# Optimization experiments

Measured on AMD Instinct MI355X. Metric: run time of the kernel, lower is better.

## Reference

```python
import jax, jax.numpy as jnp
import numpy as np

N_NODES = 50000
N_EDGES = 600000
EMB_DIM = 128
NUM_LAYERS = 5
NUM_ELEM = 118
NUM_CHIR = 4
NUM_BOND_TYPE = 4
NUM_BOND_DIR = 3
BN_EPS = 1e-5


def _xavier(key, shape):
    fan_in, fan_out = shape[0], shape[1]
    limit = np.sqrt(6.0 / (fan_in + fan_out))
    return jax.random.uniform(key, shape, jnp.float32, -limit, limit)


def setup_inputs() -> dict:
    key = jax.random.key(0)
    ks = jax.random.split(key, 12)
    x = jax.random.randint(ks[0], (N_NODES, 2), 0, 4, dtype=jnp.int64)
    edge_index = jax.random.randint(ks[1], (2, N_EDGES), 0, N_NODES, dtype=jnp.int64)
    edge_attr = jax.random.randint(ks[2], (N_EDGES, 2), 0, 3, dtype=jnp.int64)
    elem_emb = _xavier(ks[3], (NUM_ELEM, EMB_DIM))
    chir_emb = _xavier(ks[4], (NUM_CHIR, EMB_DIM))
    bond_type_emb = _xavier(ks[5], (NUM_BOND_TYPE, EMB_DIM))
    bond_dir_emb = _xavier(ks[6], (NUM_BOND_DIR, EMB_DIM))
    # shared GINEConv MLP: Linear(D, 2D) -> ReLU -> Linear(2D, D)
    W1 = _xavier(ks[7], (EMB_DIM, 2 * EMB_DIM))
    b1 = jnp.zeros((2 * EMB_DIM,), jnp.float32)
    W2 = _xavier(ks[8], (2 * EMB_DIM, EMB_DIM))
    b2 = jnp.zeros((EMB_DIM,), jnp.float32)
    # per-layer BatchNorm affine params
    bn_gamma = jnp.ones((NUM_LAYERS, EMB_DIM), jnp.float32)
    bn_beta = jnp.zeros((NUM_LAYERS, EMB_DIM), jnp.float32)
    return {
        "x": x, "edge_index": edge_index, "edge_attr": edge_attr,
        "elem_emb": elem_emb, "chir_emb": chir_emb,
        "bond_type_emb": bond_type_emb, "bond_dir_emb": bond_dir_emb,
        "W1": W1, "b1": b1, "W2": W2, "b2": b2,
        "bn_gamma": bn_gamma, "bn_beta": bn_beta,
    }


def reference(x, edge_index, edge_attr, elem_emb, chir_emb,
              bond_type_emb, bond_dir_emb, W1, b1, W2, b2,
              bn_gamma, bn_beta):
    # input embeddings
    h = elem_emb[x[:, 0]] + chir_emb[x[:, 1]]                    # [N, D]
    e = bond_type_emb[edge_attr[:, 0]] + bond_dir_emb[edge_attr[:, 1]]  # [E, D]
    src, dst = edge_index[0], edge_index[1]
    n = h.shape[0]
    num_layers = bn_gamma.shape[0]
    for layer in range(num_layers):  # conv weights shared across layers
        # GINEConv: msg = relu(x_j + edge_attr), scatter-add, eps=0
        msg = jax.nn.relu(h[src] + e)                            # [E, D]
        agg = jax.ops.segment_sum(msg, dst, num_segments=n)      # [N, D]
        z = h + agg
        out = jax.nn.relu(z @ W1 + b1) @ W2 + b2                 # [N, D]
        # BatchNorm1d (training mode: batch stats, biased variance)
        mean = out.mean(axis=0)
        var = out.var(axis=0)
        out = (out - mean) * jax.lax.rsqrt(var + BN_EPS) * bn_gamma[layer] + bn_beta[layer]
        h = out if layer == num_layers - 1 else jax.nn.relu(out)
    return h
```

## Files before the change

kernel.cpp:

```cpp
#include <hip/hip_runtime.h>

typedef _Float16 f16;
typedef _Float16 f16x8 __attribute__((ext_vector_type(8)));
typedef _Float16 h2 __attribute__((ext_vector_type(2)));
typedef float f32x4 __attribute__((ext_vector_type(4)));
typedef unsigned short u16;
typedef unsigned int u32;

__device__ __forceinline__ float bf2f(u16 b) {
  union { u32 u; float f; } t; t.u = ((u32)b) << 16; return t.f;
}
__device__ __forceinline__ u16 f2bf(float f) {
  union { float f; u32 u; } t; t.f = f;
  u32 u = t.u;
  return (u16)((u + 0x7FFFu + ((u >> 16) & 1u)) >> 16);
}
__device__ __forceinline__ u16 f2h_bits(float f) {
  f16 h = (f16)f;
  union { f16 h; u16 u; } t; t.h = h; return t.u;
}
__device__ __forceinline__ float2 up2(u32 p) {
  union { u32 u; f16 h[2]; } t; t.u = p;
  float2 r; r.x = (float)t.h[0]; r.y = (float)t.h[1]; return r;
}
__device__ __forceinline__ u32 pk2(float x, float y) {
  return (u32)f2h_bits(x) | ((u32)f2h_bits(y) << 16);
}
__device__ __forceinline__ h2 asH2(u32 u) {
  union { u32 u; h2 h; } t; t.u = u; return t.h;
}
__device__ __forceinline__ h2 relu2(h2 a) {
#if __has_builtin(__builtin_elementwise_max)
  h2 z = {(_Float16)0, (_Float16)0};
  return __builtin_elementwise_max(a, z);
#else
  h2 r;
  r.x = a.x > (_Float16)0 ? a.x : (_Float16)0;
  r.y = a.y > (_Float16)0 ? a.y : (_Float16)0;
  return r;
#endif
}

__global__ void k_detect(const u16* __restrict__ elemRaw, const int* __restrict__ eiRaw,
                         int* __restrict__ dflags) {
  __shared__ int bad, nzOdd;
  if (threadIdx.x == 0) { bad = 0; nzOdd = 0; }
  __syncthreads();
  int myBad = 0;
  for (int i = threadIdx.x; i < 4096; i += 256) {
    float v = bf2f(elemRaw[i]);
    if (!(v > -0.2f && v < 0.2f)) myBad++;
  }
  if (myBad) atomicAdd(&bad, myBad);
  int myNz = 0;
  for (int i = threadIdx.x; i < 1024; i += 256)
    if (eiRaw[2 * i + 1] != 0) myNz++;
  if (myNz) atomicAdd(&nzOdd, myNz);
  __syncthreads();
  if (threadIdx.x == 0) {
    dflags[0] = (bad == 0) ? 1 : 0;
    dflags[1] = (nzOdd > 16) ? 1 : 0;
  }
}

__global__ void k_init(const u16* __restrict__ elemRaw, const int* __restrict__ eiRaw,
                       int* __restrict__ dflags, int* __restrict__ counts,
                       float* __restrict__ statsC, int NPad, int statsZ) {
  if (blockIdx.x == 0) {
    __shared__ int bad, nzOdd;
    if (threadIdx.x == 0) { bad = 0; nzOdd = 0; }
    __syncthreads();
    int myBad = 0;
    for (int i = threadIdx.x; i < 4096; i += 256) {
      float v = bf2f(elemRaw[i]);
      if (!(v > -0.2f && v < 0.2f)) myBad++;
    }
    if (myBad) atomicAdd(&bad, myBad);
    int myNz = 0;
    for (int i = threadIdx.x; i < 1024; i += 256)
      if (eiRaw[2 * i + 1] != 0) myNz++;
    if (myNz) atomicAdd(&nzOdd, myNz);
    __syncthreads();
    if (threadIdx.x == 0) {
      dflags[0] = (bad == 0) ? 1 : 0;
      dflags[1] = (nzOdd > 16) ? 1 : 0;
    }
  } else {
    int i = (blockIdx.x - 1) * 256 + threadIdx.x;
    if (i < NPad) counts[i] = 0;
    else if (i < NPad + statsZ) statsC[i - NPad] = 0.f;
  }
}

__global__ void k_canary(u32* __restrict__ out, const int* __restrict__ dflags,
                         int out_size, u32 pBf, u32 pF32) {
  int isbf = dflags[0];
  int words = isbf ? (out_size >> 1) : out_size;
  int i = blockIdx.x * 256 + threadIdx.x;
  if (i < words) out[i] = isbf ? pBf : pF32;
}

__global__ void k_cvt(const int* __restrict__ xR, const int* __restrict__ eiR,
                      const int* __restrict__ eaR,
                      const u16* e0, const u16* e1, const u16* e2, const u16* e3,
                      const u16* e4, const u16* e5, const u16* e6, const u16* e7,
                      const u16* e8, const u16* e9,
                      const int* __restrict__ dflags,
                      int* __restrict__ x32, int* __restrict__ ei32, int* __restrict__ combo,
                      int* __restrict__ counts, float* __restrict__ dst,
                      int N, int E, int intBlocks) {
  if ((int)blockIdx.x < intBlocks) {
    int pi = blockIdx.x * 256 + threadIdx.x;
    int nPairs = N + 2 * E;
    if (pi >= nPairs) return;
    int is32 = dflags[1];
    const int* src; int local; int kind;
    if (pi < N) { src = xR; local = pi; kind = 0; }
    else if (pi < N + E) { src = eiR; local = pi - N; kind = 1; }
    else { src = eaR; local = pi - N - E; kind = 2; }
    int j0 = 2 * local;
    int v0, v1;
    if (is32) { int2 v = *(const int2*)(src + j0); v0 = v.x; v1 = v.y; }
    else      { int4 v = *(const int4*)(src + 2 * j0); v0 = v.x; v1 = v.z; }
    if (kind == 0) { x32[j0] = v0; x32[j0 + 1] = v1; }
    else if (kind == 1) {
      ei32[j0] = v0; ei32[j0 + 1] = v1;
      if (j0 >= E) {
        atomicAdd(&counts[v0], 1);
        atomicAdd(&counts[v1], 1);
      }
    } else {
      combo[local] = v0 * 3 + v1;
    }
  } else {
    int i = (blockIdx.x - intBlocks) * 256 + threadIdx.x;
    if (i >= 83712) return;
    int isbf = dflags[0];
    const u16* src; int j;
    if      (i < 15104) { src = e0; j = i; }
    else if (i < 15616) { src = e1; j = i - 15104; }
    else if (i < 16128) { src = e2; j = i - 15616; }
    else if (i < 16512) { src = e3; j = i - 16128; }
    else if (i < 49280) { src = e4; j = i - 16512; }
    else if (i < 49536) { src = e5; j = i - 49280; }
    else if (i < 82304) { src = e6; j = i - 49536; }
    else if (i < 82432) { src = e7; j = i - 82304; }
    else if (i < 83072) { src = e8; j = i - 82432; }
    else                { src = e9; j = i - 83072; }
    dst[i] = isbf ? bf2f(src[j]) : ((const float*)src)[j];
  }
}

__global__ void k_chunksum(const int* __restrict__ counts, int* __restrict__ bsum) {
  int tid = threadIdx.x, lane = tid & 63, w = tid >> 6;
  const int4* c4 = (const int4*)(counts + blockIdx.x * 1024);
  int4 v = c4[tid];
  int s = v.x + v.y + v.z + v.w;
#pragma unroll
  for (int d = 1; d < 64; d <<= 1) s += __shfl_xor(s, d);
  __shared__ int ws[4];
  if (lane == 0) ws[w] = s;
  __syncthreads();
  if (tid == 0) bsum[blockIdx.x] = ws[0] + ws[1] + ws[2] + ws[3];
}

__global__ void k_chunkscan(const int* __restrict__ bsum, int* __restrict__ boff,
                            int* __restrict__ row_start, int N, int nCh) {
  int t = threadIdx.x;
  int v = (t < nCh) ? bsum[t] : 0;
  int incl = v;
#pragma unroll
  for (int d = 1; d < 64; d <<= 1) { int tmp = __shfl_up(incl, d); if (t >= d) incl += tmp; }
  boff[t] = incl - v;
  if (t == 63) row_start[N] = incl;
}

__global__ void k_scanapply(const int* __restrict__ counts, const int* __restrict__ boff,
                            int* __restrict__ row_start, int* __restrict__ cursor, int N) {
  int tid = threadIdx.x, lane = tid & 63, w = tid >> 6;
  int base = blockIdx.x * 1024 + tid * 4;
  int4 v = *(const int4*)(counts + base);
  int tsum = v.x + v.y + v.z + v.w;
  int incl = tsum;
#pragma unroll
  for (int d = 1; d < 64; d <<= 1) { int tmp = __shfl_up(incl, d); if (lane >= d) incl += tmp; }
  __shared__ int ws[4];
  if (lane == 63) ws[w] = incl;
  __syncthreads();
  int woff = 0;
  for (int j = 0; j < w; ++j) woff += ws[j];
  int excl = boff[blockIdx.x] + woff + incl - tsum;
  int e0 = excl, e1 = excl + v.x, e2 = e1 + v.y, e3 = e2 + v.z;
  if (base < N)     { row_start[base] = e0;     cursor[base] = e0; }
  if (base + 1 < N) { row_start[base + 1] = e1; cursor[base + 1] = e1; }
  if (base + 2 < N) { row_start[base + 2] = e2; cursor[base + 2] = e2; }
  if (base + 3 < N) { row_start[base + 3] = e3; cursor[base + 3] = e3; }
}

__global__ void k_scatter(const int* __restrict__ ei, const int* __restrict__ combo,
                          int* cursor, int* packed, int E) {
  int e = blockIdx.x * blockDim.x + threadIdx.x;
  if (e >= E) return;
  int s = ei[e], d = ei[E + e];
  int cb = combo[e];
  int pos = atomicAdd(&cursor[d], 1);
  packed[pos] = s | (cb << 20);
}

__global__ void k_prep(const float* __restrict__ cflt, const int* __restrict__ x,
                       u32* __restrict__ W1F, u32* __restrict__ W2F,
                       u32* __restrict__ tblC, u32* __restrict__ hb, int N, int wtBlocks) {
  if ((int)blockIdx.x < wtBlocks) {
    const float* W1 = cflt + 16512;
    const float* W2 = cflt + 49536;
    const float* bt = cflt + 15616;
    const float* bd = cflt + 16128;
    int g = blockIdx.x * 256 + threadIdx.x;
    {
      int e = g >> 2, wd = g & 3;
      int lane = e & 63, nt = (e >> 6) & 3, ks = (e >> 8) & 3, c = (e >> 10) & 3;
      int q = lane >> 4, lo = lane & 15;
      int n = c * 64 + nt * 16 + lo;
      int k0 = (ks * 4 + q) * 8 + wd * 2;
      W1F[g] = pk2(W1[k0 * 256 + n], W1[(k0 + 1) * 256 + n]);
    }
    {
      int e = g >> 2, wd = g & 3;
      int lane = e & 63, nt = (e >> 6) & 7, ks2 = (e >> 9) & 1, c = (e >> 10) & 3;
      int q = lane >> 4, lo = lane & 15;
      int n2 = nt * 16 + lo;
      int k20 = c * 64 + (ks2 * 4 + q) * 8 + wd * 2;
      W2F[g] = pk2(W2[k20 * 128 + n2], W2[(k20 + 1) * 128 + n2]);
    }
    if (g < 768) {
      int combo = g >> 6, l = g & 63, c0 = l * 2;
      int a0 = combo / 3, a1 = combo - a0 * 3;
      tblC[g] = pk2(bt[a0 * 128 + c0] + bd[a1 * 128 + c0],
                    bt[a0 * 128 + c0 + 1] + bd[a1 * 128 + c0 + 1]);
    }
  } else {
    const float* elem = cflt;
    const float* chir = cflt + 15104;
    int b = blockIdx.x - wtBlocks;
    int wv = (int)(threadIdx.x >> 6);
    int lane = threadIdx.x & 63;
    int node = b * 4 + wv;
    if (node >= N) return;
    int x0 = x[node * 2], x1 = x[node * 2 + 1];
    int c0 = lane * 2;
    float vx = elem[x0 * 128 + c0] + chir[x1 * 128 + c0];
    float vy = elem[x0 * 128 + c0 + 1] + chir[x1 * 128 + c0 + 1];
    hb[(size_t)node * 64 + lane] = pk2(vx, vy);
  }
}

__global__ __launch_bounds__(256) void k_agg(
    const u32* __restrict__ hb, const int* __restrict__ row_start,
    const int* __restrict__ packed, const u32* __restrict__ tblC,
    u32* __restrict__ z, int N) {
  __shared__ u32 tbl[768];
  for (int idx = threadIdx.x; idx < 768; idx += 256) tbl[idx] = tblC[idx];
  __syncthreads();
  const uint4* tbl4 = (const uint4*)tbl;
  const int tid = threadIdx.x;
  const int w = tid >> 6, lane = tid & 63;
  const int sub = lane >> 4, li = lane & 15;
  const int node = blockIdx.x * 16 + w * 4 + sub;
  if (node >= N) return;
  const uint4* hb4 = (const uint4*)hb;
  uint4 sv = hb4[(size_t)node * 16 + li];
  float2 s0 = up2(sv.x), s1 = up2(sv.y), s2 = up2(sv.z), s3 = up2(sv.w);
  float ax0 = s0.x, ay0 = s0.y, ax1 = s1.x, ay1 = s1.y;
  float ax2 = s2.x, ay2 = s2.y, ax3 = s3.x, ay3 = s3.y;
  const int s_ = row_start[node], e_ = row_start[node + 1];
  int p = s_;
  for (; p + 4 <= e_; p += 4) {
    int k0 = packed[p], k1 = packed[p + 1], k2 = packed[p + 2], k3 = packed[p + 3];
    uint4 r0 = hb4[(size_t)(k0 & 0xFFFFF) * 16 + li];
    uint4 r1 = hb4[(size_t)(k1 & 0xFFFFF) * 16 + li];
    uint4 r2 = hb4[(size_t)(k2 & 0xFFFFF) * 16 + li];
    uint4 r3 = hb4[(size_t)(k3 & 0xFFFFF) * 16 + li];
    uint4 t0 = tbl4[(k0 >> 20) * 16 + li];
    uint4 t1 = tbl4[(k1 >> 20) * 16 + li];
    uint4 t2 = tbl4[(k2 >> 20) * 16 + li];
    uint4 t3 = tbl4[(k3 >> 20) * 16 + li];
    h2 m;
    m = relu2(asH2(r0.x) + asH2(t0.x)); ax0 += (float)m.x; ay0 += (float)m.y;
    m = relu2(asH2(r0.y) + asH2(t0.y)); ax1 += (float)m.x; ay1 += (float)m.y;
    m = relu2(asH2(r0.z) + asH2(t0.z)); ax2 += (float)m.x; ay2 += (float)m.y;
    m = relu2(asH2(r0.w) + asH2(t0.w)); ax3 += (float)m.x; ay3 += (float)m.y;
    m = relu2(asH2(r1.x) + asH2(t1.x)); ax0 += (float)m.x; ay0 += (float)m.y;
    m = relu2(asH2(r1.y) + asH2(t1.y)); ax1 += (float)m.x; ay1 += (float)m.y;
    m = relu2(asH2(r1.z) + asH2(t1.z)); ax2 += (float)m.x; ay2 += (float)m.y;
    m = relu2(asH2(r1.w) + asH2(t1.w)); ax3 += (float)m.x; ay3 += (float)m.y;
    m = relu2(asH2(r2.x) + asH2(t2.x)); ax0 += (float)m.x; ay0 += (float)m.y;
    m = relu2(asH2(r2.y) + asH2(t2.y)); ax1 += (float)m.x; ay1 += (float)m.y;
    m = relu2(asH2(r2.z) + asH2(t2.z)); ax2 += (float)m.x; ay2 += (float)m.y;
    m = relu2(asH2(r2.w) + asH2(t2.w)); ax3 += (float)m.x; ay3 += (float)m.y;
    m = relu2(asH2(r3.x) + asH2(t3.x)); ax0 += (float)m.x; ay0 += (float)m.y;
    m = relu2(asH2(r3.y) + asH2(t3.y)); ax1 += (float)m.x; ay1 += (float)m.y;
    m = relu2(asH2(r3.z) + asH2(t3.z)); ax2 += (float)m.x; ay2 += (float)m.y;
    m = relu2(asH2(r3.w) + asH2(t3.w)); ax3 += (float)m.x; ay3 += (float)m.y;
  }
  for (; p < e_; ++p) {
    int k0 = packed[p];
    uint4 r0 = hb4[(size_t)(k0 & 0xFFFFF) * 16 + li];
    uint4 t0 = tbl4[(k0 >> 20) * 16 + li];
    h2 m;
    m = relu2(asH2(r0.x) + asH2(t0.x)); ax0 += (float)m.x; ay0 += (float)m.y;
    m = relu2(asH2(r0.y) + asH2(t0.y)); ax1 += (float)m.x; ay1 += (float)m.y;
    m = relu2(asH2(r0.z) + asH2(t0.z)); ax2 += (float)m.x; ay2 += (float)m.y;
    m = relu2(asH2(r0.w) + asH2(t0.w)); ax3 += (float)m.x; ay3 += (float)m.y;
  }
  uint4 o;
  o.x = pk2(ax0, ay0); o.y = pk2(ax1, ay1); o.z = pk2(ax2, ay2); o.w = pk2(ax3, ay3);
  ((uint4*)z)[(size_t)node * 16 + li] = o;
}

__global__ __launch_bounds__(512, 2) void k_mlp(
    const u16* __restrict__ z, const u32* __restrict__ W1F, const u32* __restrict__ W2F,
    const float* __restrict__ b1, const float* __restrict__ b2,
    u16* __restrict__ act, float* __restrict__ statsC, int N, int nTiles) {
  __shared__ u32 sW1[16384];
  __shared__ u32 sW2[16384];
  __shared__ u16 sYp[8][1024];
  __shared__ float sStats[256];

  const int tid = threadIdx.x;
  const int w = tid >> 6, lane = tid & 63;
  const int lo = lane & 15, q = lane >> 4;

  if (tid < 256) sStats[tid] = 0.f;
  {
    const int4* gW1 = (const int4*)W1F;
    const int4* gW2 = (const int4*)W2F;
    int4* lW1 = (int4*)sW1;
    int4* lW2 = (int4*)sW2;
#pragma unroll
    for (int it = 0; it < 8; ++it) {
      int o = it * 512 + tid;
      lW1[o] = gW1[o];
      lW2[o] = gW2[o];
    }
  }
  __syncthreads();

  float rb1[16], rb2[8];
#pragma unroll
  for (int c = 0; c < 4; ++c)
#pragma unroll
    for (int nt = 0; nt < 4; ++nt)
      rb1[c * 4 + nt] = b1[c * 64 + nt * 16 + lo];
#pragma unroll
  for (int nt = 0; nt < 8; ++nt)
    rb2[nt] = b2[nt * 16 + lo];

  float aSum[8] = {}, aSq[8] = {};
  u16* myY = sYp[w];

  for (int t = blockIdx.x * 8 + w; t < nTiles; t += 2048) {
    const int row0 = t * 16;
    f16x8 a1[4];
    const char* zrow = (const char*)z + (size_t)(row0 + lo) * 256;
#pragma unroll
    for (int ks = 0; ks < 4; ++ks)
      a1[ks] = *(const f16x8*)(zrow + (ks * 4 + q) * 16);

    f32x4 accO[8] = {};
#pragma unroll
    for (int c = 0; c < 4; ++c) {
      f16x8 B1[16];
#pragma unroll
      for (int i = 0; i < 16; ++i)
        B1[i] = *(const f16x8*)((const char*)sW1 + ((c * 16 + i) << 10) + lane * 16);
      f32x4 acc1[4] = {};
#pragma unroll
      for (int ks = 0; ks < 4; ++ks)
#pragma unroll
        for (int nt = 0; nt < 4; ++nt)
          acc1[nt] = __builtin_amdgcn_mfma_f32_16x16x32_f16(a1[ks], B1[ks * 4 + nt], acc1[nt], 0, 0, 0);
#pragma unroll
      for (int nt = 0; nt < 4; ++nt) {
        int ycol = nt * 16 + lo;
        float bias = rb1[c * 4 + nt];
#pragma unroll
        for (int i = 0; i < 4; ++i) {
          int m = q * 4 + i;
          float v = fmaxf(acc1[nt][i] + bias, 0.f);
          myY[m * 64 + (((ycol >> 3) ^ (m & 7)) << 3) + (ycol & 7)] = f2h_bits(v);
        }
      }
      f16x8 B2[16];
#pragma unroll
      for (int i = 0; i < 16; ++i)
        B2[i] = *(const f16x8*)((const char*)sW2 + ((c * 16 + i) << 10) + lane * 16);
#pragma unroll
      for (int ks2 = 0; ks2 < 2; ++ks2) {
        int kq2 = ks2 * 4 + q;
        f16x8 a2 = *(const f16x8*)(myY + lo * 64 + ((kq2 ^ (lo & 7)) << 3));
#pragma unroll
        for (int nt = 0; nt < 8; ++nt)
          accO[nt] = __builtin_amdgcn_mfma_f32_16x16x32_f16(a2, B2[ks2 * 8 + nt], accO[nt], 0, 0, 0);
      }
    }
#pragma unroll
    for (int nt = 0; nt < 8; ++nt) {
      int n2 = nt * 16 + lo;
      float bias = rb2[nt];
#pragma unroll
      for (int i = 0; i < 4; ++i) {
        int row = row0 + q * 4 + i;
        float v = accO[nt][i] + bias;
        act[(size_t)row * 128 + n2] = f2h_bits(v);
        if (row < N) { aSum[nt] += v; aSq[nt] += v * v; }
      }
    }
  }

#pragma unroll
  for (int nt = 0; nt < 8; ++nt) {
    float s = aSum[nt], s2 = aSq[nt];
    s += __shfl_xor(s, 16); s += __shfl_xor(s, 32);
    s2 += __shfl_xor(s2, 16); s2 += __shfl_xor(s2, 32);
    if (q == 0) {
      atomicAdd(&sStats[nt * 16 + lo], s);
      atomicAdd(&sStats[128 + nt * 16 + lo], s2);
    }
  }
  __syncthreads();
  if (tid < 256) atomicAdd(&statsC[(blockIdx.x & 31) * 256 + tid], sStats[tid]);
}

__global__ __launch_bounds__(256) void k_bnapply(
    const u32* __restrict__ act, const float* __restrict__ statsC,
    const float* __restrict__ gamma, const float* __restrict__ beta,
    float invN, u32* __restrict__ hb, int N) {
  __shared__ float sTot[256];
  __shared__ float ssc[128], ssh[128];
  int tid = threadIdx.x;
  {
    float acc = 0.f;
#pragma unroll
    for (int c = 0; c < 32; ++c) acc += statsC[c * 256 + tid];
    sTot[tid] = acc;
  }
  __syncthreads();
  if (tid < 128) {
    float mean = sTot[tid] * invN;
    float var = sTot[128 + tid] * invN - mean * mean;
    float inv = rsqrtf(var + 1e-5f);
    float scv = gamma[tid] * inv;
    ssc[tid] = scv;
    ssh[tid] = beta[tid] - mean * scv;
  }
  __syncthreads();
  int total = N * 64;
  for (int i = blockIdx.x * 256 + tid; i < total; i += gridDim.x * 256) {
    int c0 = (i & 63) * 2;
    float2 v = up2(act[i]);
    float ox = fmaxf(v.x * ssc[c0] + ssh[c0], 0.f);
    float oy = fmaxf(v.y * ssc[c0 + 1] + ssh[c0 + 1], 0.f);
    hb[i] = pk2(ox, oy);
  }
}

__global__ __launch_bounds__(256) void k_final(
    const u32* __restrict__ act, const float* __restrict__ statsC,
    const float* __restrict__ gamma, const float* __restrict__ beta,
    float invN, const int* __restrict__ dflags, void* __restrict__ outv, int N) {
  __shared__ float sTot[256];
  __shared__ float ssc[128], ssh[128];
  int tid = threadIdx.x;
  {
    float acc = 0.f;
#pragma unroll
    for (int c = 0; c < 32; ++c) acc += statsC[c * 256 + tid];
    sTot[tid] = acc;
  }
  __syncthreads();
  if (tid < 128) {
    float mean = sTot[tid] * invN;
    float var = sTot[128 + tid] * invN - mean * mean;
    float inv = rsqrtf(var + 1e-5f);
    float scv = gamma[tid] * inv;
    ssc[tid] = scv;
    ssh[tid] = beta[tid] - mean * scv;
  }
  __syncthreads();
  int isbf = dflags[0];
  int total = N * 64;
  for (int i = blockIdx.x * 256 + tid; i < total; i += gridDim.x * 256) {
    int c0 = (i & 63) * 2;
    float2 v = up2(act[i]);
    float ox = v.x * ssc[c0] + ssh[c0];
    float oy = v.y * ssc[c0 + 1] + ssh[c0 + 1];
    if (isbf) ((u32*)outv)[i] = (u32)f2bf(ox) | ((u32)f2bf(oy) << 16);
    else { float2 o; o.x = ox; o.y = oy; ((float2*)outv)[i] = o; }
  }
}

extern "C" void kernel_launch(void* const* d_in, const int* in_sizes, int n_in,
                              void* d_out, int out_size, void* d_ws, size_t ws_size,
                              hipStream_t stream) {
  const int* xR  = (const int*)d_in[0];
  const int* eiR = (const int*)d_in[1];
  const int* eaR = (const int*)d_in[2];
  const u16* emR = (const u16*)d_in[3];
  const u16* chR = (const u16*)d_in[4];
  const u16* btR = (const u16*)d_in[5];
  const u16* bdR = (const u16*)d_in[6];
  const u16* W1R = (const u16*)d_in[7];
  const u16* b1R = (const u16*)d_in[8];
  const u16* W2R = (const u16*)d_in[9];
  const u16* b2R = (const u16*)d_in[10];
  const u16* gR  = (const u16*)d_in[11];
  const u16* beR = (const u16*)d_in[12];

  const int N = in_sizes[0] / 2;
  const int E = in_sizes[1] / 2;
  const int L = in_sizes[11] / 128;
  const int Mpad = ((N + 63) / 64) * 64;
  const int nCh = (N + 1023) / 1024;
  const int NPad = nCh * 1024;
  const int nTiles = (N + 15) / 16;

  char* base = (char*)d_ws;
  size_t off = 0;
  auto take = [&](size_t bytes) -> void* {
    void* p = base + off;
    off += (bytes + 255) & ~(size_t)255;
    return p;
  };
  int*   dflags    = (int*)  take(256);
  int*   x32       = (int*)  take((size_t)2 * N * 4);
  int*   ei32      = (int*)  take((size_t)2 * E * 4);
  int*   combo     = (int*)  take((size_t)E * 4);
  float* cflt      = (float*)take(83712 * 4);
  u32*   act       = (u32*)  take((size_t)Mpad * 64 * 4);
  u32*   hb        = (u32*)  take((size_t)Mpad * 64 * 4);
  u16*   zb        = (u16*)  take((size_t)Mpad * 128 * 2);
  int*   packed    = (int*)  take((size_t)E * 4);
  int*   row_start = (int*)  take((size_t)(N + 1) * 4);
  int*   cursor    = (int*)  take((size_t)N * 4);
  int*   counts    = (int*)  take((size_t)NPad * 4);
  int*   bsum      = (int*)  take(64 * 4);
  int*   boff      = (int*)  take(64 * 4);
  float* statsC    = (float*)take((size_t)L * 32 * 256 * 4);
  u32*   W1F       = (u32*)  take(16384 * 4);
  u32*   W2F       = (u32*)  take(16384 * 4);
  u32*   tblC      = (u32*)  take(768 * 4);
  const size_t need = off;
  (void)n_in;

  float* cB1 = cflt + 49280;
  float* cB2 = cflt + 82304;
  float* cGamma = cflt + 82432;
  float* cBeta = cflt + 83072;

  if (need > ws_size) {
    k_detect<<<dim3(1), dim3(256), 0, stream>>>(emR, eiR, dflags);
    k_canary<<<dim3((out_size + 255) / 256), dim3(256), 0, stream>>>(
        (u32*)d_out, dflags, out_size, 0x40004000u, 0x40000000u);
    return;
  }

  const int statsZ = L * 32 * 256;
  const int nzBlocks = (NPad + statsZ + 255) / 256;
  k_init<<<dim3(nzBlocks + 1), dim3(256), 0, stream>>>(emR, eiR, dflags, counts, statsC,
                                                       NPad, statsZ);

  const int nPairs = N + 2 * E;
  const int intBlocks = (nPairs + 255) / 256;
  const int fltBlocks = (83712 + 255) / 256;
  k_cvt<<<dim3(intBlocks + fltBlocks), dim3(256), 0, stream>>>(
      xR, eiR, eaR, emR, chR, btR, bdR, W1R, b1R, W2R, b2R, gR, beR,
      dflags, x32, ei32, combo, counts, cflt, N, E, intBlocks);

  k_chunksum<<<dim3(nCh), dim3(256), 0, stream>>>(counts, bsum);
  k_chunkscan<<<dim3(1), dim3(64), 0, stream>>>(bsum, boff, row_start, N, nCh);
  k_scanapply<<<dim3(nCh), dim3(256), 0, stream>>>(counts, boff, row_start, cursor, N);
  k_scatter<<<dim3((E + 255) / 256), dim3(256), 0, stream>>>(ei32, combo, cursor, packed, E);

  const int wtBlocks = 64;
  k_prep<<<dim3(wtBlocks + (N + 3) / 4), dim3(256), 0, stream>>>(
      cflt, x32, W1F, W2F, tblC, hb, N, wtBlocks);

  const float invN = 1.0f / (float)N;
  for (int l = 0; l < L; ++l) {
    k_agg<<<dim3((N + 15) / 16), dim3(256), 0, stream>>>(
        hb, row_start, packed, tblC, (u32*)zb, N);
    k_mlp<<<dim3(256), dim3(512), 0, stream>>>(
        zb, W1F, W2F, cB1, cB2, (u16*)act, statsC + (size_t)l * 32 * 256, N, nTiles);
    if (l < L - 1) {
      k_bnapply<<<dim3(1024), dim3(256), 0, stream>>>(
          act, statsC + (size_t)l * 32 * 256, cGamma + (size_t)l * 128,
          cBeta + (size_t)l * 128, invN, hb, N);
    }
  }
  k_final<<<dim3(1024), dim3(256), 0, stream>>>(
      act, statsC + (size_t)(L - 1) * 32 * 256, cGamma + (size_t)(L - 1) * 128,
      cBeta + (size_t)(L - 1) * 128, invN, dflags, d_out, N);
}
```

Measured before the change: 451.1 us.

## Process aggregation nodes in degree-sorted order to balance per-wave work

```diff
diff --git a/kernel.cpp b/kernel.cpp
--- a/kernel.cpp
+++ b/kernel.cpp
@@ -65,7 +65,8 @@
 
 __global__ void k_init(const u16* __restrict__ elemRaw, const int* __restrict__ eiRaw,
                        int* __restrict__ dflags, int* __restrict__ counts,
-                       float* __restrict__ statsC, int NPad, int statsZ) {
+                       float* __restrict__ statsC, int* __restrict__ dhist,
+                       int NPad, int statsZ) {
   if (blockIdx.x == 0) {
     __shared__ int bad, nzOdd;
     if (threadIdx.x == 0) { bad = 0; nzOdd = 0; }
@@ -89,6 +90,7 @@
     int i = (blockIdx.x - 1) * 256 + threadIdx.x;
     if (i < NPad) counts[i] = 0;
     else if (i < NPad + statsZ) statsC[i - NPad] = 0.f;
+    else if (i < NPad + statsZ + 64) dhist[i - NPad - statsZ] = 0;
   }
 }
 
@@ -151,42 +153,75 @@
   }
 }
 
-__global__ void k_chunksum(const int* __restrict__ counts, int* __restrict__ bsum) {
+__global__ void k_chunksum(const int* __restrict__ counts, int* __restrict__ bsum,
+                           int* __restrict__ dhist, int N) {
   int tid = threadIdx.x, lane = tid & 63, w = tid >> 6;
+  __shared__ int lh[64];
+  __shared__ int ws[4];
+  if (tid < 64) lh[tid] = 0;
+  __syncthreads();
   const int4* c4 = (const int4*)(counts + blockIdx.x * 1024);
   int4 v = c4[tid];
+  int base = blockIdx.x * 1024 + tid * 4;
+  if (base < N)     atomicAdd(&lh[min(v.x, 63)], 1);
+  if (base + 1 < N) atomicAdd(&lh[min(v.y, 63)], 1);
+  if (base + 2 < N) atomicAdd(&lh[min(v.z, 63)], 1);
+  if (base + 3 < N) atomicAdd(&lh[min(v.w, 63)], 1);
   int s = v.x + v.y + v.z + v.w;
 #pragma unroll
   for (int d = 1; d < 64; d <<= 1) s += __shfl_xor(s, d);
+  if (lane == 0) ws[w] = s;
+  __syncthreads();
+  if (tid == 0) bsum[blockIdx.x] = ws[0] + ws[1] + ws[2] + ws[3];
+  if (tid < 64 && lh[tid]) atomicAdd(&dhist[tid], lh[tid]);
+}
+
+__global__ void k_chunkscan(const int* __restrict__ bsum, int* __restrict__ boff,
+                            int* __restrict__ row_start, const int* __restrict__ dhist,
+                            int* __restrict__ dcur, int N, int nCh) {
+  int tid = threadIdx.x;
+  if (tid < 64) {
+    int t = tid;
+    int v = (t < nCh) ? bsum[t] : 0;
+    int incl = v;
+#pragma unroll
+    for (int d = 1; d < 64; d <<= 1) { int tmp = __shfl_up(incl, d); if (t >= d) incl += tmp; }
+    boff[t] = incl - v;
+    if (t == 63) row_start[N] = incl;
+  } else {
+    int t = tid - 64;
+    int v = dhist[t];
+    int incl = v;
+#pragma unroll
+    for (int d = 1; d < 64; d <<= 1) { int tmp = __shfl_up(incl, d); if (t >= d) incl += tmp; }
+    dcur[t] = incl - v;
+  }
+}
+
+__global__ void k_scanapply(const int* __restrict__ counts, const int* __restrict__ boff,
+                            int* __restrict__ row_start, int* __restrict__ cursor,
+                            int* __restrict__ dcur, int* __restrict__ order, int N) {
+  int tid = threadIdx.x, lane = tid & 63, w = tid >> 6;
+  __shared__ int lh[64];
+  __shared__ int lb[64];
   __shared__ int ws[4];
-  if (lane == 0) ws[w] = s;
-  __syncthreads();
-  if (tid == 0) bsum[blockIdx.x] = ws[0] + ws[1] + ws[2] + ws[3];
-}
-
-__global__ void k_chunkscan(const int* __restrict__ bsum, int* __restrict__ boff,
-                            int* __restrict__ row_start, int N, int nCh) {
-  int t = threadIdx.x;
-  int v = (t < nCh) ? bsum[t] : 0;
-  int incl = v;
-#pragma unroll
-  for (int d = 1; d < 64; d <<= 1) { int tmp = __shfl_up(incl, d); if (t >= d) incl += tmp; }
-  boff[t] = incl - v;
-  if (t == 63) row_start[N] = incl;
-}
-
-__global__ void k_scanapply(const int* __restrict__ counts, const int* __restrict__ boff,
-                            int* __restrict__ row_start, int* __restrict__ cursor, int N) {
-  int tid = threadIdx.x, lane = tid & 63, w = tid >> 6;
+  if (tid < 64) lh[tid] = 0;
+  __syncthreads();
   int base = blockIdx.x * 1024 + tid * 4;
   int4 v = *(const int4*)(counts + base);
+  int d0 = min(v.x, 63), d1 = min(v.y, 63), d2 = min(v.z, 63), d3 = min(v.w, 63);
+  int o0 = 0, o1 = 0, o2 = 0, o3 = 0;
+  if (base < N)     o0 = atomicAdd(&lh[d0], 1);
+  if (base + 1 < N) o1 = atomicAdd(&lh[d1], 1);
+  if (base + 2 < N) o2 = atomicAdd(&lh[d2], 1);
+  if (base + 3 < N) o3 = atomicAdd(&lh[d3], 1);
   int tsum = v.x + v.y + v.z + v.w;
   int incl = tsum;
 #pragma unroll
   for (int d = 1; d < 64; d <<= 1) { int tmp = __shfl_up(incl, d); if (lane >= d) incl += tmp; }
-  __shared__ int ws[4];
   if (lane == 63) ws[w] = incl;
   __syncthreads();
+  if (tid < 64) lb[tid] = lh[tid] ? atomicAdd(&dcur[tid], lh[tid]) : 0;
   int woff = 0;
   for (int j = 0; j < w; ++j) woff += ws[j];
   int excl = boff[blockIdx.x] + woff + incl - tsum;
@@ -195,6 +230,11 @@
   if (base + 1 < N) { row_start[base + 1] = e1; cursor[base + 1] = e1; }
   if (base + 2 < N) { row_start[base + 2] = e2; cursor[base + 2] = e2; }
   if (base + 3 < N) { row_start[base + 3] = e3; cursor[base + 3] = e3; }
+  __syncthreads();
+  if (base < N)     order[lb[d0] + o0] = base;
+  if (base + 1 < N) order[lb[d1] + o1] = base + 1;
+  if (base + 2 < N) order[lb[d2] + o2] = base + 2;
+  if (base + 3 < N) order[lb[d3] + o3] = base + 3;
 }
 
 __global__ void k_scatter(const int* __restrict__ ei, const int* __restrict__ combo,
@@ -257,6 +297,7 @@
 __global__ __launch_bounds__(256) void k_agg(
     const u32* __restrict__ hb, const int* __restrict__ row_start,
     const int* __restrict__ packed, const u32* __restrict__ tblC,
+    const int* __restrict__ order,
     u32* __restrict__ z, int N) {
   __shared__ u32 tbl[768];
   for (int idx = threadIdx.x; idx < 768; idx += 256) tbl[idx] = tblC[idx];
@@ -265,8 +306,9 @@
   const int tid = threadIdx.x;
   const int w = tid >> 6, lane = tid & 63;
   const int sub = lane >> 4, li = lane & 15;
-  const int node = blockIdx.x * 16 + w * 4 + sub;
-  if (node >= N) return;
+  const int nidx = blockIdx.x * 16 + w * 4 + sub;
+  if (nidx >= N) return;
+  const int node = order[nidx];
   const uint4* hb4 = (const uint4*)hb;
   uint4 sv = hb4[(size_t)node * 16 + li];
   float2 s0 = up2(sv.x), s1 = up2(sv.y), s2 = up2(sv.z), s3 = up2(sv.w);
@@ -549,6 +591,9 @@
   u32*   W1F       = (u32*)  take(16384 * 4);
   u32*   W2F       = (u32*)  take(16384 * 4);
   u32*   tblC      = (u32*)  take(768 * 4);
+  int*   order     = (int*)  take((size_t)N * 4);
+  int*   dhist     = (int*)  take(64 * 4);
+  int*   dcur      = (int*)  take(64 * 4);
   const size_t need = off;
   (void)n_in;
 
@@ -565,9 +610,9 @@
   }
 
   const int statsZ = L * 32 * 256;
-  const int nzBlocks = (NPad + statsZ + 255) / 256;
+  const int nzBlocks = (NPad + statsZ + 64 + 255) / 256;
   k_init<<<dim3(nzBlocks + 1), dim3(256), 0, stream>>>(emR, eiR, dflags, counts, statsC,
-                                                       NPad, statsZ);
+                                                       dhist, NPad, statsZ);
 
   const int nPairs = N + 2 * E;
   const int intBlocks = (nPairs + 255) / 256;
@@ -576,9 +621,10 @@
       xR, eiR, eaR, emR, chR, btR, bdR, W1R, b1R, W2R, b2R, gR, beR,
       dflags, x32, ei32, combo, counts, cflt, N, E, intBlocks);
 
-  k_chunksum<<<dim3(nCh), dim3(256), 0, stream>>>(counts, bsum);
-  k_chunkscan<<<dim3(1), dim3(64), 0, stream>>>(bsum, boff, row_start, N, nCh);
-  k_scanapply<<<dim3(nCh), dim3(256), 0, stream>>>(counts, boff, row_start, cursor, N);
+  k_chunksum<<<dim3(nCh), dim3(256), 0, stream>>>(counts, bsum, dhist, N);
+  k_chunkscan<<<dim3(1), dim3(128), 0, stream>>>(bsum, boff, row_start, dhist, dcur, N, nCh);
+  k_scanapply<<<dim3(nCh), dim3(256), 0, stream>>>(counts, boff, row_start, cursor,
+                                                   dcur, order, N);
   k_scatter<<<dim3((E + 255) / 256), dim3(256), 0, stream>>>(ei32, combo, cursor, packed, E);
 
   const int wtBlocks = 64;
@@ -588,7 +634,7 @@
   const float invN = 1.0f / (float)N;
   for (int l = 0; l < L; ++l) {
     k_agg<<<dim3((N + 15) / 16), dim3(256), 0, stream>>>(
-        hb, row_start, packed, tblC, (u32*)zb, N);
+        hb, row_start, packed, tblC, order, (u32*)zb, N);
     k_mlp<<<dim3(256), dim3(512), 0, stream>>>(
         zb, W1F, W2F, cB1, cB2, (u16*)act, statsC + (size_t)l * 32 * 256, N, nTiles);
     if (l < L - 1) {
```

Measured after the change: 451.9 us. Within noise of the previous version (+0.2%).

## Fuse per-layer agg, MLP and batchnorm into one cooperative persistent kernel

Applied to the files above, without the earlier changes.

```diff
diff --git a/kernel.cpp b/kernel.cpp
--- a/kernel.cpp
+++ b/kernel.cpp
@@ -1,4 +1,7 @@
 #include <hip/hip_runtime.h>
+#include <hip/hip_cooperative_groups.h>
+
+namespace cg = cooperative_groups;
 
 typedef _Float16 f16;
 typedef _Float16 f16x8 __attribute__((ext_vector_type(8)));
@@ -254,6 +257,225 @@
   }
 }
 
+
+__device__ __forceinline__ void agg_body(
+    const u32* __restrict__ hb, const int* __restrict__ row_start,
+    const int* __restrict__ packed, const uint4* __restrict__ tbl4,
+    u32* __restrict__ z, int N, int bid, int nb, int w, int lane) {
+  const int sub = lane >> 4, li = lane & 15;
+  const uint4* hb4 = (const uint4*)hb;
+#define ACC4(R, T)                                                              \
+  {                                                                             \
+    h2 m;                                                                       \
+    m = relu2(asH2((R).x) + asH2((T).x)); ax0 += (float)m.x; ay0 += (float)m.y; \
+    m = relu2(asH2((R).y) + asH2((T).y)); ax1 += (float)m.x; ay1 += (float)m.y; \
+    m = relu2(asH2((R).z) + asH2((T).z)); ax2 += (float)m.x; ay2 += (float)m.y; \
+    m = relu2(asH2((R).w) + asH2((T).w)); ax3 += (float)m.x; ay3 += (float)m.y; \
+  }
+  for (int base = bid * 32; base < N; base += nb * 32) {
+    const int node = base + w * 4 + sub;
+    if (node >= N) continue;
+    uint4 sv = hb4[(size_t)node * 16 + li];
+    float2 s0 = up2(sv.x), s1 = up2(sv.y), s2 = up2(sv.z), s3 = up2(sv.w);
+    float ax0 = s0.x, ay0 = s0.y, ax1 = s1.x, ay1 = s1.y;
+    float ax2 = s2.x, ay2 = s2.y, ax3 = s3.x, ay3 = s3.y;
+    const int s_ = row_start[node], e_ = row_start[node + 1];
+    int p = s_;
+    for (; p + 4 <= e_; p += 4) {
+      int k0 = packed[p], k1 = packed[p + 1], k2 = packed[p + 2], k3 = packed[p + 3];
+      uint4 r0 = hb4[(size_t)(k0 & 0xFFFFF) * 16 + li];
+      uint4 r1 = hb4[(size_t)(k1 & 0xFFFFF) * 16 + li];
+      uint4 r2 = hb4[(size_t)(k2 & 0xFFFFF) * 16 + li];
+      uint4 r3 = hb4[(size_t)(k3 & 0xFFFFF) * 16 + li];
+      uint4 t;
+      t = tbl4[(k0 >> 20) * 16 + li]; ACC4(r0, t)
+      t = tbl4[(k1 >> 20) * 16 + li]; ACC4(r1, t)
+      t = tbl4[(k2 >> 20) * 16 + li]; ACC4(r2, t)
+      t = tbl4[(k3 >> 20) * 16 + li]; ACC4(r3, t)
+    }
+    for (; p < e_; ++p) {
+      int k0 = packed[p];
+      uint4 r0 = hb4[(size_t)(k0 & 0xFFFFF) * 16 + li];
+      uint4 t = tbl4[(k0 >> 20) * 16 + li];
+      ACC4(r0, t)
+    }
+    uint4 o;
+    o.x = pk2(ax0, ay0); o.y = pk2(ax1, ay1); o.z = pk2(ax2, ay2); o.w = pk2(ax3, ay3);
+    ((uint4*)z)[(size_t)node * 16 + li] = o;
+  }
+#undef ACC4
+}
+
+__global__ __launch_bounds__(512, 1) void k_fused(
+    u32* hb, u32* zb, u32* act,
+    const int* row_start, const int* packed,
+    const u32* tblC, const u32* W1F, const u32* W2F,
+    const float* b1, const float* b2,
+    const float* gamma, const float* beta, float* statsC,
+    const int* dflags, void* outv,
+    int N, int nTiles, int L, float invN) {
+  __shared__ u32 sW1[16384];
+  __shared__ u32 sW2[16384];
+  __shared__ u16 sYp[8][1024];
+  __shared__ float sStats[256];
+  __shared__ u32 tbl[768];
+  __shared__ float ssc[128], ssh[128];
+
+  cg::grid_group grid = cg::this_grid();
+
+  const int tid = threadIdx.x;
+  const int w = tid >> 6, lane = tid & 63;
+  const int lo = lane & 15, q = lane >> 4;
+  const int bid = blockIdx.x, nb = gridDim.x;
+
+  {
+    const int4* gW1 = (const int4*)W1F;
+    const int4* gW2 = (const int4*)W2F;
+    int4* lW1 = (int4*)sW1;
+    int4* lW2 = (int4*)sW2;
+    for (int o = tid; o < 4096; o += 512) { lW1[o] = gW1[o]; lW2[o] = gW2[o]; }
+    for (int idx = tid; idx < 768; idx += 512) tbl[idx] = tblC[idx];
+  }
+  float rb1[16], rb2[8];
+#pragma unroll
+  for (int c = 0; c < 4; ++c)
+#pragma unroll
+    for (int nt = 0; nt < 4; ++nt)
+      rb1[c * 4 + nt] = b1[c * 64 + nt * 16 + lo];
+#pragma unroll
+  for (int nt = 0; nt < 8; ++nt)
+    rb2[nt] = b2[nt * 16 + lo];
+  __syncthreads();
+
+  u16* myY = sYp[w];
+
+  for (int l = 0; l < L; ++l) {
+    agg_body(hb, row_start, packed, (const uint4*)tbl, zb, N, bid, nb, w, lane);
+    grid.sync();
+
+    if (tid < 256) sStats[tid] = 0.f;
+    __syncthreads();
+    {
+      float aSum[8] = {}, aSq[8] = {};
+      const u16* z16 = (const u16*)zb;
+      for (int t = bid * 8 + w; t < nTiles; t += nb * 8) {
+        const int row0 = t * 16;
+        f16x8 a1[4];
+        const char* zrow = (const char*)z16 + (size_t)(row0 + lo) * 256;
+#pragma unroll
+        for (int ks = 0; ks < 4; ++ks)
+          a1[ks] = *(const f16x8*)(zrow + (ks * 4 + q) * 16);
+
+        f32x4 accO[8] = {};
+#pragma unroll
+        for (int c = 0; c < 4; ++c) {
+          f16x8 B1[16];
+#pragma unroll
+          for (int i = 0; i < 16; ++i)
+            B1[i] = *(const f16x8*)((const char*)sW1 + ((c * 16 + i) << 10) + lane * 16);
+          f32x4 acc1[4] = {};
+#pragma unroll
+          for (int ks = 0; ks < 4; ++ks)
+#pragma unroll
+            for (int nt = 0; nt < 4; ++nt)
+              acc1[nt] = __builtin_amdgcn_mfma_f32_16x16x32_f16(a1[ks], B1[ks * 4 + nt], acc1[nt], 0, 0, 0);
+#pragma unroll
+          for (int nt = 0; nt < 4; ++nt) {
+            int ycol = nt * 16 + lo;
+            float bias = rb1[c * 4 + nt];
+#pragma unroll
+            for (int i = 0; i < 4; ++i) {
+              int m = q * 4 + i;
+              float v = fmaxf(acc1[nt][i] + bias, 0.f);
+              myY[m * 64 + (((ycol >> 3) ^ (m & 7)) << 3) + (ycol & 7)] = f2h_bits(v);
+            }
+          }
+          f16x8 B2[16];
+#pragma unroll
+          for (int i = 0; i < 16; ++i)
+            B2[i] = *(const f16x8*)((const char*)sW2 + ((c * 16 + i) << 10) + lane * 16);
+#pragma unroll
+          for (int ks2 = 0; ks2 < 2; ++ks2) {
+            int kq2 = ks2 * 4 + q;
+            f16x8 a2 = *(const f16x8*)(myY + lo * 64 + ((kq2 ^ (lo & 7)) << 3));
+#pragma unroll
+            for (int nt = 0; nt < 8; ++nt)
+              accO[nt] = __builtin_amdgcn_mfma_f32_16x16x32_f16(a2, B2[ks2 * 8 + nt], accO[nt], 0, 0, 0);
+          }
+        }
+#pragma unroll
+        for (int nt = 0; nt < 8; ++nt) {
+          int n2 = nt * 16 + lo;
+          float bias = rb2[nt];
+#pragma unroll
+          for (int i = 0; i < 4; ++i) {
+            int row = row0 + q * 4 + i;
+            float v = accO[nt][i] + bias;
+            ((u16*)act)[(size_t)row * 128 + n2] = f2h_bits(v);
+            if (row < N) { aSum[nt] += v; aSq[nt] += v * v; }
+          }
+        }
+      }
+#pragma unroll
+      for (int nt = 0; nt < 8; ++nt) {
+        float s = aSum[nt], s2 = aSq[nt];
+        s += __shfl_xor(s, 16); s += __shfl_xor(s, 32);
+        s2 += __shfl_xor(s2, 16); s2 += __shfl_xor(s2, 32);
+        if (q == 0) {
+          atomicAdd(&sStats[nt * 16 + lo], s);
+          atomicAdd(&sStats[128 + nt * 16 + lo], s2);
+        }
+      }
+      __syncthreads();
+      float* scl = statsC + (size_t)l * 32 * 256;
+      if (tid < 256) atomicAdd(&scl[(bid & 31) * 256 + tid], sStats[tid]);
+    }
+    grid.sync();
+
+    {
+      const float* scl = statsC + (size_t)l * 32 * 256;
+      if (tid < 256) {
+        float acc = 0.f;
+#pragma unroll
+        for (int c = 0; c < 32; ++c) acc += scl[c * 256 + tid];
+        sStats[tid] = acc;
+      }
+      __syncthreads();
+      if (tid < 128) {
+        float mean = sStats[tid] * invN;
+        float var = sStats[128 + tid] * invN - mean * mean;
+        float inv = rsqrtf(var + 1e-5f);
+        float scv = gamma[l * 128 + tid] * inv;
+        ssc[tid] = scv;
+        ssh[tid] = beta[l * 128 + tid] - mean * scv;
+      }
+      __syncthreads();
+      int total = N * 64;
+      if (l < L - 1) {
+        for (int i = bid * 512 + tid; i < total; i += nb * 512) {
+          int c0 = (i & 63) * 2;
+          float2 v = up2(act[i]);
+          float ox = fmaxf(v.x * ssc[c0] + ssh[c0], 0.f);
+          float oy = fmaxf(v.y * ssc[c0 + 1] + ssh[c0 + 1], 0.f);
+          hb[i] = pk2(ox, oy);
+        }
+        grid.sync();
+      } else {
+        int isbf = dflags[0];
+        for (int i = bid * 512 + tid; i < total; i += nb * 512) {
+          int c0 = (i & 63) * 2;
+          float2 v = up2(act[i]);
+          float ox = v.x * ssc[c0] + ssh[c0];
+          float oy = v.y * ssc[c0 + 1] + ssh[c0 + 1];
+          if (isbf) ((u32*)outv)[i] = (u32)f2bf(ox) | ((u32)f2bf(oy) << 16);
+          else { float2 o2; o2.x = ox; o2.y = oy; ((float2*)outv)[i] = o2; }
+        }
+      }
+    }
+  }
+}
+
+
 __global__ __launch_bounds__(256) void k_agg(
     const u32* __restrict__ hb, const int* __restrict__ row_start,
     const int* __restrict__ packed, const u32* __restrict__ tblC,
@@ -261,60 +483,9 @@
   __shared__ u32 tbl[768];
   for (int idx = threadIdx.x; idx < 768; idx += 256) tbl[idx] = tblC[idx];
   __syncthreads();
-  const uint4* tbl4 = (const uint4*)tbl;
   const int tid = threadIdx.x;
   const int w = tid >> 6, lane = tid & 63;
-  const int sub = lane >> 4, li = lane & 15;
-  const int node = blockIdx.x * 16 + w * 4 + sub;
-  if (node >= N) return;
-  const uint4* hb4 = (const uint4*)hb;
-  uint4 sv = hb4[(size_t)node * 16 + li];
-  float2 s0 = up2(sv.x), s1 = up2(sv.y), s2 = up2(sv.z), s3 = up2(sv.w);
-  float ax0 = s0.x, ay0 = s0.y, ax1 = s1.x, ay1 = s1.y;
-  float ax2 = s2.x, ay2 = s2.y, ax3 = s3.x, ay3 = s3.y;
-  const int s_ = row_start[node], e_ = row_start[node + 1];
-  int p = s_;
-  for (; p + 4 <= e_; p += 4) {
-    int k0 = packed[p], k1 = packed[p + 1], k2 = packed[p + 2], k3 = packed[p + 3];
-    uint4 r0 = hb4[(size_t)(k0 & 0xFFFFF) * 16 + li];
-    uint4 r1 = hb4[(size_t)(k1 & 0xFFFFF) * 16 + li];
-    uint4 r2 = hb4[(size_t)(k2 & 0xFFFFF) * 16 + li];
-    uint4 r3 = hb4[(size_t)(k3 & 0xFFFFF) * 16 + li];
-    uint4 t0 = tbl4[(k0 >> 20) * 16 + li];
-    uint4 t1 = tbl4[(k1 >> 20) * 16 + li];
-    uint4 t2 = tbl4[(k2 >> 20) * 16 + li];
-    uint4 t3 = tbl4[(k3 >> 20) * 16 + li];
-    h2 m;
-    m = relu2(asH2(r0.x) + asH2(t0.x)); ax0 += (float)m.x; ay0 += (float)m.y;
-    m = relu2(asH2(r0.y) + asH2(t0.y)); ax1 += (float)m.x; ay1 += (float)m.y;
-    m = relu2(asH2(r0.z) + asH2(t0.z)); ax2 += (float)m.x; ay2 += (float)m.y;
-    m = relu2(asH2(r0.w) + asH2(t0.w)); ax3 += (float)m.x; ay3 += (float)m.y;
-    m = relu2(asH2(r1.x) + asH2(t1.x)); ax0 += (float)m.x; ay0 += (float)m.y;
-    m = relu2(asH2(r1.y) + asH2(t1.y)); ax1 += (float)m.x; ay1 += (float)m.y;
-    m = relu2(asH2(r1.z) + asH2(t1.z)); ax2 += (float)m.x; ay2 += (float)m.y;
-    m = relu2(asH2(r1.w) + asH2(t1.w)); ax3 += (float)m.x; ay3 += (float)m.y;
-    m = relu2(asH2(r2.x) + asH2(t2.x)); ax0 += (float)m.x; ay0 += (float)m.y;
-    m = relu2(asH2(r2.y) + asH2(t2.y)); ax1 += (float)m.x; ay1 += (float)m.y;
-    m = relu2(asH2(r2.z) + asH2(t2.z)); ax2 += (float)m.x; ay2 += (float)m.y;
-    m = relu2(asH2(r2.w) + asH2(t2.w)); ax3 += (float)m.x; ay3 += (float)m.y;
-    m = relu2(asH2(r3.x) + asH2(t3.x)); ax0 += (float)m.x; ay0 += (float)m.y;
-    m = relu2(asH2(r3.y) + asH2(t3.y)); ax1 += (float)m.x; ay1 += (float)m.y;
-    m = relu2(asH2(r3.z) + asH2(t3.z)); ax2 += (float)m.x; ay2 += (float)m.y;
-    m = relu2(asH2(r3.w) + asH2(t3.w)); ax3 += (float)m.x; ay3 += (float)m.y;
-  }
-  for (; p < e_; ++p) {
-    int k0 = packed[p];
-    uint4 r0 = hb4[(size_t)(k0 & 0xFFFFF) * 16 + li];
-    uint4 t0 = tbl4[(k0 >> 20) * 16 + li];
-    h2 m;
-    m = relu2(asH2(r0.x) + asH2(t0.x)); ax0 += (float)m.x; ay0 += (float)m.y;
-    m = relu2(asH2(r0.y) + asH2(t0.y)); ax1 += (float)m.x; ay1 += (float)m.y;
-    m = relu2(asH2(r0.z) + asH2(t0.z)); ax2 += (float)m.x; ay2 += (float)m.y;
-    m = relu2(asH2(r0.w) + asH2(t0.w)); ax3 += (float)m.x; ay3 += (float)m.y;
-  }
-  uint4 o;
-  o.x = pk2(ax0, ay0); o.y = pk2(ax1, ay1); o.z = pk2(ax2, ay2); o.w = pk2(ax3, ay3);
-  ((uint4*)z)[(size_t)node * 16 + li] = o;
+  agg_body(hb, row_start, packed, (const uint4*)tbl, z, N, blockIdx.x, gridDim.x, w, lane);
 }
 
 __global__ __launch_bounds__(512, 2) void k_mlp(
@@ -533,7 +704,7 @@
   };
   int*   dflags    = (int*)  take(256);
   int*   x32       = (int*)  take((size_t)2 * N * 4);
-  int*   ei32      = (int*)  take((size_t)2 * E * 4);
+  int*   ei32     = (int*)  take((size_t)2 * E * 4);
   int*   combo     = (int*)  take((size_t)E * 4);
   float* cflt      = (float*)take(83712 * 4);
   u32*   act       = (u32*)  take((size_t)Mpad * 64 * 4);
@@ -586,8 +757,36 @@
       cflt, x32, W1F, W2F, tblC, hb, N, wtBlocks);
 
   const float invN = 1.0f / (float)N;
+
+  {
+    u32* zb32 = (u32*)zb;
+    void* outp = d_out;
+    const int* rsC = row_start;
+    const int* pkC = packed;
+    const u32* tblCC = tblC;
+    const u32* W1C = W1F;
+    const u32* W2C = W2F;
+    const float* b1C = cB1;
+    const float* b2C = cB2;
+    const float* gC = cGamma;
+    const float* beC = cBeta;
+    const int* dfC = dflags;
+    int Nv = N, nTv = nTiles, Lv = L;
+    float invNv = invN;
+    void* kargs[] = {
+        (void*)&hb, (void*)&zb32, (void*)&act,
+        (void*)&rsC, (void*)&pkC, (void*)&tblCC, (void*)&W1C, (void*)&W2C,
+        (void*)&b1C, (void*)&b2C, (void*)&gC, (void*)&beC, (void*)&statsC,
+        (void*)&dfC, (void*)&outp,
+        (void*)&Nv, (void*)&nTv, (void*)&Lv, (void*)&invNv};
+    hipError_t err = hipLaunchCooperativeKernel(
+        (void*)k_fused, dim3(256), dim3(512), kargs, 0, stream);
+    if (err == hipSuccess) return;
+    (void)hipGetLastError();
+  }
+
   for (int l = 0; l < L; ++l) {
-    k_agg<<<dim3((N + 15) / 16), dim3(256), 0, stream>>>(
+    k_agg<<<dim3((N + 31) / 32), dim3(256), 0, stream>>>(
         hb, row_start, packed, tblC, (u32*)zb, N);
     k_mlp<<<dim3(256), dim3(512), 0, stream>>>(
         zb, W1F, W2F, cB1, cB2, (u16*)act, statsC + (size_t)l * 32 * 256, N, nTiles);
```

Result: slower. 945.8 us (+109.7%).

## Fuse MLP and BatchNorm apply into one cooperative kernel with grid sync

Applied to the files above, without the earlier changes.

```diff
diff --git a/kernel.cpp b/kernel.cpp
--- a/kernel.cpp
+++ b/kernel.cpp
@@ -1,4 +1,7 @@
 #include <hip/hip_runtime.h>
+#include <hip/hip_cooperative_groups.h>
+
+namespace cg = cooperative_groups;
 
 typedef _Float16 f16;
 typedef _Float16 f16x8 __attribute__((ext_vector_type(8)));
@@ -317,48 +320,13 @@
   ((uint4*)z)[(size_t)node * 16 + li] = o;
 }
 
-__global__ __launch_bounds__(512, 2) void k_mlp(
-    const u16* __restrict__ z, const u32* __restrict__ W1F, const u32* __restrict__ W2F,
-    const float* __restrict__ b1, const float* __restrict__ b2,
-    u16* __restrict__ act, float* __restrict__ statsC, int N, int nTiles) {
-  __shared__ u32 sW1[16384];
-  __shared__ u32 sW2[16384];
-  __shared__ u16 sYp[8][1024];
-  __shared__ float sStats[256];
-
-  const int tid = threadIdx.x;
-  const int w = tid >> 6, lane = tid & 63;
-  const int lo = lane & 15, q = lane >> 4;
-
-  if (tid < 256) sStats[tid] = 0.f;
-  {
-    const int4* gW1 = (const int4*)W1F;
-    const int4* gW2 = (const int4*)W2F;
-    int4* lW1 = (int4*)sW1;
-    int4* lW2 = (int4*)sW2;
-#pragma unroll
-    for (int it = 0; it < 8; ++it) {
-      int o = it * 512 + tid;
-      lW1[o] = gW1[o];
-      lW2[o] = gW2[o];
-    }
-  }
-  __syncthreads();
-
-  float rb1[16], rb2[8];
-#pragma unroll
-  for (int c = 0; c < 4; ++c)
-#pragma unroll
-    for (int nt = 0; nt < 4; ++nt)
-      rb1[c * 4 + nt] = b1[c * 64 + nt * 16 + lo];
-#pragma unroll
-  for (int nt = 0; nt < 8; ++nt)
-    rb2[nt] = b2[nt * 16 + lo];
-
+__device__ __forceinline__ void mlp_body(
+    const u16* __restrict__ z, const u32* sW1, const u32* sW2,
+    const float* rb1, const float* rb2, u16* myY,
+    u16* __restrict__ act, float* sStats, float* __restrict__ statsCl,
+    int N, int nTiles, int bid, int nb, int w, int lane, int lo, int q, int tid) {
   float aSum[8] = {}, aSq[8] = {};
-  u16* myY = sYp[w];
-
-  for (int t = blockIdx.x * 8 + w; t < nTiles; t += 2048) {
+  for (int t = bid * 8 + w; t < nTiles; t += nb * 8) {
     const int row0 = t * 16;
     f16x8 a1[4];
     const char* zrow = (const char*)z + (size_t)(row0 + lo) * 256;
@@ -416,7 +384,6 @@
       }
     }
   }
-
 #pragma unroll
   for (int nt = 0; nt < 8; ++nt) {
     float s = aSum[nt], s2 = aSq[nt];
@@ -428,7 +395,138 @@
     }
   }
   __syncthreads();
-  if (tid < 256) atomicAdd(&statsC[(blockIdx.x & 31) * 256 + tid], sStats[tid]);
+  if (tid < 256) atomicAdd(&statsCl[(bid & 31) * 256 + tid], sStats[tid]);
+}
+
+__global__ __launch_bounds__(512, 1) void k_mlpbn(
+    const u16* z, const u32* W1F, const u32* W2F,
+    const float* b1, const float* b2,
+    u16* act, float* statsCl,
+    const float* gamma, const float* beta, float invN,
+    u32* hb, const int* dflags, void* outv, int isFinal, int N, int nTiles) {
+  __shared__ u32 sW1[16384];
+  __shared__ u32 sW2[16384];
+  __shared__ u16 sYp[8][1024];
+  __shared__ float sStats[256];
+  __shared__ float ssc[128], ssh[128];
+
+  cg::grid_group grid = cg::this_grid();
+
+  const int tid = threadIdx.x;
+  const int w = tid >> 6, lane = tid & 63;
+  const int lo = lane & 15, q = lane >> 4;
+  const int bid = blockIdx.x, nb = gridDim.x;
+
+  if (tid < 256) sStats[tid] = 0.f;
+  {
+    const int4* gW1 = (const int4*)W1F;
+    const int4* gW2 = (const int4*)W2F;
+    int4* lW1 = (int4*)sW1;
+    int4* lW2 = (int4*)sW2;
+#pragma unroll
+    for (int it = 0; it < 8; ++it) {
+      int o = it * 512 + tid;
+      lW1[o] = gW1[o];
+      lW2[o] = gW2[o];
+    }
+  }
+  __syncthreads();
+
+  float rb1[16], rb2[8];
+#pragma unroll
+  for (int c = 0; c < 4; ++c)
+#pragma unroll
+    for (int nt = 0; nt < 4; ++nt)
+      rb1[c * 4 + nt] = b1[c * 64 + nt * 16 + lo];
+#pragma unroll
+  for (int nt = 0; nt < 8; ++nt)
+    rb2[nt] = b2[nt * 16 + lo];
+
+  mlp_body(z, sW1, sW2, rb1, rb2, sYp[w], act, sStats, statsCl,
+           N, nTiles, bid, nb, w, lane, lo, q, tid);
+
+  grid.sync();
+
+  if (tid < 256) {
+    float acc = 0.f;
+#pragma unroll
+    for (int c = 0; c < 32; ++c) acc += statsCl[c * 256 + tid];
+    sStats[tid] = acc;
+  }
+  __syncthreads();
+  if (tid < 128) {
+    float mean = sStats[tid] * invN;
+    float var = sStats[128 + tid] * invN - mean * mean;
+    float inv = rsqrtf(var + 1e-5f);
+    float scv = gamma[tid] * inv;
+    ssc[tid] = scv;
+    ssh[tid] = beta[tid] - mean * scv;
+  }
+  __syncthreads();
+  const u32* act32 = (const u32*)act;
+  int total = N * 64;
+  if (!isFinal) {
+    for (int i = bid * 512 + tid; i < total; i += nb * 512) {
+      int c0 = (i & 63) * 2;
+      float2 v = up2(act32[i]);
+      float ox = fmaxf(v.x * ssc[c0] + ssh[c0], 0.f);
+      float oy = fmaxf(v.y * ssc[c0 + 1] + ssh[c0 + 1], 0.f);
+      hb[i] = pk2(ox, oy);
+    }
+  } else {
+    int isbf = dflags[0];
+    for (int i = bid * 512 + tid; i < total; i += nb * 512) {
+      int c0 = (i & 63) * 2;
+      float2 v = up2(act32[i]);
+      float ox = v.x * ssc[c0] + ssh[c0];
+      float oy = v.y * ssc[c0 + 1] + ssh[c0 + 1];
+      if (isbf) ((u32*)outv)[i] = (u32)f2bf(ox) | ((u32)f2bf(oy) << 16);
+      else { float2 o2; o2.x = ox; o2.y = oy; ((float2*)outv)[i] = o2; }
+    }
+  }
+}
+
+
+__global__ __launch_bounds__(512, 2) void k_mlp(
+    const u16* __restrict__ z, const u32* __restrict__ W1F, const u32* __restrict__ W2F,
+    const float* __restrict__ b1, const float* __restrict__ b2,
+    u16* __restrict__ act, float* __restrict__ statsCl, int N, int nTiles) {
+  __shared__ u32 sW1[16384];
+  __shared__ u32 sW2[16384];
+  __shared__ u16 sYp[8][1024];
+  __shared__ float sStats[256];
+
+  const int tid = threadIdx.x;
+  const int w = tid >> 6, lane = tid & 63;
+  const int lo = lane & 15, q = lane >> 4;
+
+  if (tid < 256) sStats[tid] = 0.f;
+  {
+    const int4* gW1 = (const int4*)W1F;
+    const int4* gW2 = (const int4*)W2F;
+    int4* lW1 = (int4*)sW1;
+    int4* lW2 = (int4*)sW2;
+#pragma unroll
+    for (int it = 0; it < 8; ++it) {
+      int o = it * 512 + tid;
+      lW1[o] = gW1[o];
+      lW2[o] = gW2[o];
+    }
+  }
+  __syncthreads();
+
+  float rb1[16], rb2[8];
+#pragma unroll
+  for (int c = 0; c < 4; ++c)
+#pragma unroll
+    for (int nt = 0; nt < 4; ++nt)
+      rb1[c * 4 + nt] = b1[c * 64 + nt * 16 + lo];
+#pragma unroll
+  for (int nt = 0; nt < 8; ++nt)
+    rb2[nt] = b2[nt * 16 + lo];
+
+  mlp_body(z, sW1, sW2, rb1, rb2, sYp[w], act, sStats, statsCl,
+           N, nTiles, blockIdx.x, gridDim.x, w, lane, lo, q, tid);
 }
 
 __global__ __launch_bounds__(256) void k_bnapply(
@@ -586,18 +684,48 @@
       cflt, x32, W1F, W2F, tblC, hb, N, wtBlocks);
 
   const float invN = 1.0f / (float)N;
+  bool coop = true;
   for (int l = 0; l < L; ++l) {
     k_agg<<<dim3((N + 15) / 16), dim3(256), 0, stream>>>(
         hb, row_start, packed, tblC, (u32*)zb, N);
-    k_mlp<<<dim3(256), dim3(512), 0, stream>>>(
-        zb, W1F, W2F, cB1, cB2, (u16*)act, statsC + (size_t)l * 32 * 256, N, nTiles);
-    if (l < L - 1) {
-      k_bnapply<<<dim3(1024), dim3(256), 0, stream>>>(
-          act, statsC + (size_t)l * 32 * 256, cGamma + (size_t)l * 128,
-          cBeta + (size_t)l * 128, invN, hb, N);
-    }
-  }
-  k_final<<<dim3(1024), dim3(256), 0, stream>>>(
-      act, statsC + (size_t)(L - 1) * 32 * 256, cGamma + (size_t)(L - 1) * 128,
-      cBeta + (size_t)(L - 1) * 128, invN, dflags, d_out, N);
-}
+    float* statsCl = statsC + (size_t)l * 32 * 256;
+    const float* gammaL = cGamma + (size_t)l * 128;
+    const float* betaL = cBeta + (size_t)l * 128;
+    int isFinal = (l == L - 1) ? 1 : 0;
+    if (coop) {
+      const u16* zC = (const u16*)zb;
+      u16* actC = (u16*)act;
+      const u32* W1C = W1F;
+      const u32* W2C = W2F;
+      const float* b1C = cB1;
+      const float* b2C = cB2;
+      const int* dfC = dflags;
+      void* outp = d_out;
+      u32* hbC = hb;
+      float invNv = invN;
+      int Nv = N, nTv = nTiles;
+      void* kargs[] = {
+          (void*)&zC, (void*)&W1C, (void*)&W2C, (void*)&b1C, (void*)&b2C,
+          (void*)&actC, (void*)&statsCl, (void*)&gammaL, (void*)&betaL,
+          (void*)&invNv, (void*)&hbC, (void*)&dfC, (void*)&outp,
+          (void*)&isFinal, (void*)&Nv, (void*)&nTv};
+      hipError_t err = hipLaunchCooperativeKernel(
+          (void*)k_mlpbn, dim3(256), dim3(512), kargs, 0, stream);
+      if (err != hipSuccess) {
+        (void)hipGetLastError();
+        coop = false;
+      }
+    }
+    if (!coop) {
+      k_mlp<<<dim3(256), dim3(512), 0, stream>>>(
+          zb, W1F, W2F, cB1, cB2, (u16*)act, statsCl, N, nTiles);
+      if (!isFinal) {
+        k_bnapply<<<dim3(1024), dim3(256), 0, stream>>>(
+            act, statsCl, gammaL, betaL, invN, hb, N);
+      } else {
+        k_final<<<dim3(1024), dim3(256), 0, stream>>>(
+            act, statsCl, gammaL, betaL, invN, dflags, d_out, N);
+      }
+    }
+  }
+}
```

Result: slower. 691.1 us (+53.2%).
